# Kernel tuning notes

Hardware: AMD Instinct MI355X
Metric: run time of the kernel (lower is better)

Reference implementation:

```python
import jax, jax.numpy as jnp
import numpy as np

N_NODES = 100000
N_EDGES = 1600000
N_GRAPHS = 64
IN_DIM = 128
HID = 64
N_CLASSES = 10


def setup_inputs() -> dict:
    key = jax.random.key(0)
    ks = jax.random.split(key, 8)
    x = jax.random.normal(ks[0], (N_NODES, IN_DIM), jnp.float32)
    edge_index = jax.random.randint(ks[1], (2, N_EDGES), 0, N_NODES, jnp.int32)
    graph_id = jnp.sort(jax.random.randint(ks[2], (N_NODES,), 0, N_GRAPHS, jnp.int32))
    W1 = jax.random.normal(ks[3], (IN_DIM, HID), jnp.float32) / np.sqrt(IN_DIM)
    b1 = jnp.zeros((HID,), jnp.float32)
    W2 = jax.random.normal(ks[4], (HID, HID), jnp.float32) / np.sqrt(HID)
    b2 = jnp.zeros((HID,), jnp.float32)
    attn_W = jax.random.normal(ks[5], (HID, 1), jnp.float32) / np.sqrt(HID)
    attn_b = jnp.zeros((1,), jnp.float32)
    cls_W = jax.random.normal(ks[6], (HID, N_CLASSES), jnp.float32) / np.sqrt(HID)
    cls_b = jnp.zeros((N_CLASSES,), jnp.float32)
    return {"x": x, "edge_index": edge_index, "graph_id": graph_id,
            "W1": W1, "b1": b1, "W2": W2, "b2": b2,
            "attn_W": attn_W, "attn_b": attn_b, "cls_W": cls_W, "cls_b": cls_b}


def _graph_conv(h, W, b, src, dst, norm_out, norm_in):
    # DGL GraphConv, norm='both': D_in^{-1/2} A D_out^{-1/2} (h W) + b
    h = h @ W                                  # [N, out]
    h = h * norm_out[:, None]                  # scale by src out-degree^{-1/2}
    m = jax.ops.segment_sum(h[src], dst, num_segments=N_NODES)  # SpMM aggregation
    return m * norm_in[:, None] + b


def reference(x, edge_index, graph_id, W1, b1, W2, b2, attn_W, attn_b, cls_W, cls_b):
    src, dst = edge_index[0], edge_index[1]
    ones_e = jnp.ones((src.shape[0],), jnp.float32)
    deg_out = jnp.clip(jax.ops.segment_sum(ones_e, src, num_segments=N_NODES), 1.0)
    deg_in = jnp.clip(jax.ops.segment_sum(ones_e, dst, num_segments=N_NODES), 1.0)
    norm_out = jax.lax.rsqrt(deg_out)
    norm_in = jax.lax.rsqrt(deg_in)

    h = jax.nn.relu(_graph_conv(x, W1, b1, src, dst, norm_out, norm_in))
    h = jax.nn.relu(_graph_conv(h, W2, b2, src, dst, norm_out, norm_in))

    hw = jax.nn.sigmoid(h @ attn_W + attn_b)   # [N, 1] attention gate
    h = h * hw

    # mean_nodes: per-graph mean pooling
    sums = jax.ops.segment_sum(h, graph_id, num_segments=N_GRAPHS)        # [G, HID]
    cnts = jnp.clip(jax.ops.segment_sum(jnp.ones((N_NODES,), jnp.float32), graph_id,
                                        num_segments=N_GRAPHS), 1.0)
    hg = sums / cnts[:, None]
    out = hg @ cls_W + cls_b                   # [G, n_classes]
    return out, hw
```

## Files before the change

kernel.cpp:

```cpp
#include <hip/hip_runtime.h>
#include <stdint.h>


#define N_NODES   100000
#define N_EDGES   1600000
#define N_GRAPHS  64
#define IN_DIM    128
#define HID       64
#define N_CLASSES 10

#define NBUCK     391
#define P1B       196
#define EPB       8192
#define GB_BLOCKS 391
#define MTILES    6250
#define GEMM_BLOCKS 1563
#define SPMM_BLOCKS 3125
#define POOL_SLICES 32
#define WS_NEED   33885952u

typedef __attribute__((ext_vector_type(8))) short short8v;
typedef __attribute__((ext_vector_type(4))) float f32x4;
typedef __bf16 bf16x8 __attribute__((ext_vector_type(8)));

__device__ __forceinline__ f32x4 mfma16(short8v a, short8v b, f32x4 c) {
  return __builtin_amdgcn_mfma_f32_16x16x32_bf16(
      __builtin_bit_cast(bf16x8, a), __builtin_bit_cast(bf16x8, b), c, 0, 0, 0);
}

__device__ __forceinline__ float bf2f(unsigned short u) {
  unsigned int v = ((unsigned int)u) << 16;
  float f;
  __builtin_memcpy(&f, &v, 4);
  return f;
}

__device__ __forceinline__ unsigned short f2bf(float f) {
  unsigned int x;
  __builtin_memcpy(&x, &f, 4);
  unsigned int lsb = (x >> 16) & 1u;
  x += 0x7fffu + lsb;
  return (unsigned short)(x >> 16);
}

__device__ __forceinline__ void unpack_bf2(unsigned int u, float& lo, float& hi) {
  unsigned int a = u << 16;
  unsigned int b = u & 0xffff0000u;
  __builtin_memcpy(&lo, &a, 4);
  __builtin_memcpy(&hi, &b, 4);
}

__device__ __forceinline__ float ldf(const void* p, int i, int mode) {
  return mode ? bf2f(((const unsigned short*)p)[i]) : ((const float*)p)[i];
}

__global__ __launch_bounds__(256) void fallback_kernel(unsigned short* __restrict__ out,
                                                       int n) {
  int i = blockIdx.x * 256 + threadIdx.x;
  if (i < n) out[i] = 0;
}

__global__ __launch_bounds__(256) void wcvt_kernel(
    const unsigned short* __restrict__ xu,
    const void* __restrict__ W1, const void* __restrict__ W2,
    const void* __restrict__ b1, const void* __restrict__ b2,
    const void* __restrict__ attnW, const void* __restrict__ attnb,
    const void* __restrict__ clsW, const void* __restrict__ clsb,
    unsigned short* __restrict__ W1hf, unsigned short* __restrict__ W1lf,
    unsigned short* __restrict__ W2hf, unsigned short* __restrict__ W2lf,
    float* __restrict__ b1f, float* __restrict__ b2f,
    float* __restrict__ attnWf, float* __restrict__ attnbf,
    float* __restrict__ clsWf, float* __restrict__ clsbf,
    int* __restrict__ flag) {
  __shared__ int cnt[4];
  __shared__ int smode;
  int tid = (int)threadIdx.x;
  unsigned u = xu[2 * tid];
  int e = (int)((u >> 7) & 0xFF);
  int ok = (e >= 110 && e <= 132) ? 1 : 0;
  unsigned long long m = __ballot(ok);
  if ((tid & 63) == 0) cnt[tid >> 6] = __popcll(m);
  __syncthreads();
  if (tid == 0) {
    smode = (cnt[0] + cnt[1] + cnt[2] + cnt[3] > 128) ? 1 : 0;
    if (blockIdx.x == 0) {
      flag[0] = smode;
      flag[1] = 1;
    }
  }
  __syncthreads();
  int mode = smode;

  int i = blockIdx.x * 256 + tid;
  if (i < 1024) {
    int tile = i >> 6, lane = i & 63;
    int kt = tile >> 2, ct = tile & 3;
#pragma unroll
    for (int j = 0; j < 8; ++j) {
      int k = kt * 32 + ((lane >> 4) << 3) + j;
      int d = (ct << 4) + (lane & 15);
      float v = ldf(W1, k * HID + d, mode);
      unsigned short h = f2bf(v);
      unsigned short l = f2bf(v - bf2f(h));
      W1hf[i * 8 + j] = h;
      W1lf[i * 8 + j] = l;
    }
  } else if (i < 1536) {
    int ii = i - 1024;
    int tile = ii >> 6, lane = ii & 63;
    int kt = tile >> 2, ct = tile & 3;
#pragma unroll
    for (int j = 0; j < 8; ++j) {
      int k = kt * 32 + ((lane >> 4) << 3) + j;
      int d = (ct << 4) + (lane & 15);
      float v = ldf(W2, k * HID + d, mode);
      unsigned short h = f2bf(v);
      unsigned short l = f2bf(v - bf2f(h));
      W2hf[ii * 8 + j] = h;
      W2lf[ii * 8 + j] = l;
    }
  }
  if (i < HID) {
    b1f[i] = ldf(b1, i, mode);
    b2f[i] = ldf(b2, i, mode);
    attnWf[i] = ldf(attnW, i, mode);
  }
  if (i == 0) attnbf[0] = ldf(attnb, 0, mode);
  if (i < HID * N_CLASSES) clsWf[i] = ldf(clsW, i, mode);
  if (i < N_CLASSES) clsbf[i] = ldf(clsb, i, mode);
}

template <int K, bool SCALE>
__device__ __forceinline__ void gemm_tile(
    const void* __restrict__ A, const unsigned short* __restrict__ Whf,
    const unsigned short* __restrict__ Wlf, const float* __restrict__ norm_out,
    unsigned short* __restrict__ out, int mode, int mtile, int lane) {
  int n0 = mtile << 4;
  int row = lane & 15;
  int kg = lane >> 4;
  f32x4 acc0 = {0.f, 0.f, 0.f, 0.f};
  f32x4 acc1 = {0.f, 0.f, 0.f, 0.f};
  f32x4 acc2 = {0.f, 0.f, 0.f, 0.f};
  f32x4 acc3 = {0.f, 0.f, 0.f, 0.f};
  const short8v* whb0 = (const short8v*)Whf + lane;
  const short8v* wlb0 = (const short8v*)Wlf + lane;
  if (mode) {
    const unsigned short* xr = (const unsigned short*)A + (size_t)(n0 + row) * K + (kg << 3);
#pragma unroll
    for (int kt = 0; kt < K / 32; ++kt) {
      uint4 va = *(const uint4*)(xr + kt * 32);
      short8v xh = __builtin_bit_cast(short8v, va);
      const short8v* wh = whb0 + (size_t)(kt * 4) * 64;
      const short8v* wl = wlb0 + (size_t)(kt * 4) * 64;
      acc0 = mfma16(xh, wh[0], acc0);
      acc1 = mfma16(xh, wh[64], acc1);
      acc2 = mfma16(xh, wh[128], acc2);
      acc3 = mfma16(xh, wh[192], acc3);
      acc0 = mfma16(xh, wl[0], acc0);
      acc1 = mfma16(xh, wl[64], acc1);
      acc2 = mfma16(xh, wl[128], acc2);
      acc3 = mfma16(xh, wl[192], acc3);
    }
  } else {
    const float* xr = (const float*)A + (size_t)(n0 + row) * K + (kg << 3);
#pragma unroll
    for (int kt = 0; kt < K / 32; ++kt) {
      float4 a0 = *(const float4*)(xr + kt * 32);
      float4 a1 = *(const float4*)(xr + kt * 32 + 4);
      float xv[8] = {a0.x, a0.y, a0.z, a0.w, a1.x, a1.y, a1.z, a1.w};
      short8v xh, xl;
#pragma unroll
      for (int j = 0; j < 8; ++j) {
        unsigned short h = f2bf(xv[j]);
        unsigned short l = f2bf(xv[j] - bf2f(h));
        xh[j] = (short)h;
        xl[j] = (short)l;
      }
      const short8v* wh = whb0 + (size_t)(kt * 4) * 64;
      const short8v* wl = wlb0 + (size_t)(kt * 4) * 64;
      acc0 = mfma16(xh, wh[0], acc0);
      acc1 = mfma16(xh, wh[64], acc1);
      acc2 = mfma16(xh, wh[128], acc2);
      acc3 = mfma16(xh, wh[192], acc3);
      acc0 = mfma16(xh, wl[0], acc0);
      acc1 = mfma16(xh, wl[64], acc1);
      acc2 = mfma16(xh, wl[128], acc2);
      acc3 = mfma16(xh, wl[192], acc3);
      acc0 = mfma16(xl, wh[0], acc0);
      acc1 = mfma16(xl, wh[64], acc1);
      acc2 = mfma16(xl, wh[128], acc2);
      acc3 = mfma16(xl, wh[192], acc3);
    }
  }
  int col = lane & 15;
#pragma unroll
  for (int i = 0; i < 4; ++i) {
    int n = n0 + (kg << 2) + i;
    float s = SCALE ? norm_out[n] : 1.f;
    size_t rb = (size_t)n << 6;
    out[rb + col]      = f2bf(acc0[i] * s);
    out[rb + 16 + col] = f2bf(acc1[i] * s);
    out[rb + 32 + col] = f2bf(acc2[i] * s);
    out[rb + 48 + col] = f2bf(acc3[i] * s);
  }
}

__global__ __launch_bounds__(256) void fatA_kernel(
    const int* __restrict__ ei, int* __restrict__ blkhistD,
    int* __restrict__ blkhistS,
    const int* __restrict__ gid, int* __restrict__ gstart,
    const void* __restrict__ x, const unsigned short* __restrict__ W1hf,
    const unsigned short* __restrict__ W1lf, unsigned short* __restrict__ bufA,
    const int* __restrict__ flag) {
  int b = (int)blockIdx.x;
  int t = (int)threadIdx.x;
  if (b < P1B) {
    __shared__ int hD[NBUCK];
    __shared__ int hS[NBUCK];
    for (int i = t; i < NBUCK; i += 256) { hD[i] = 0; hS[i] = 0; }
    __syncthreads();
    int base_e = b * EPB;
    for (int s = 0; s < EPB / 1024; ++s) {
      int e4 = base_e + s * 1024 + t * 4;
      if (e4 < N_EDGES) {
        int4 s4 = *(const int4*)(ei + e4);
        int4 d4 = *(const int4*)(ei + N_EDGES + e4);
        int ss[4] = {s4.x, s4.y, s4.z, s4.w};
        int dd[4] = {d4.x, d4.y, d4.z, d4.w};
#pragma unroll
        for (int j = 0; j < 4; ++j) {
          if ((unsigned)ss[j] < N_NODES) atomicAdd(&hS[ss[j] >> 8], 1);
          if ((unsigned)dd[j] < N_NODES) atomicAdd(&hD[dd[j] >> 8], 1);
        }
      }
    }
    __syncthreads();
    for (int i = t; i < NBUCK; i += 256) {
      blkhistD[i * P1B + b] = hD[i];
      blkhistS[i * P1B + b] = hS[i];
    }
  } else if (b < P1B + GEMM_BLOCKS) {
    int mode = flag[0];
    int mtile = (b - P1B) * 4 + (t >> 6);
    if (mtile < MTILES)
      gemm_tile<IN_DIM, false>(x, W1hf, W1lf, (const float*)0, bufA, mode,
                               mtile, t & 63);
  } else {
    int bb = b - P1B - GEMM_BLOCKS;
    int n = bb * 256 + t;
    if (n >= N_NODES) return;
    int gc = gid[n] & (N_GRAPHS - 1);
    if (n == 0) {
      for (int g = 0; g <= gc; ++g) gstart[g] = 0;
    } else {
      int gp = gid[n - 1] & (N_GRAPHS - 1);
      for (int g = gp + 1; g <= gc; ++g) gstart[g] = n;
    }
    if (n == N_NODES - 1) {
      for (int g = gc + 1; g <= N_GRAPHS; ++g) gstart[g] = N_NODES;
    }
  }
}

__global__ __launch_bounds__(512) void bucket_scan_kernel(
    int* __restrict__ blkhistD, int* __restrict__ blkhistS,
    int* __restrict__ bstart_d, int* __restrict__ bstart_s) {
  int* hist = (blockIdx.x == 0) ? blkhistD : blkhistS;
  int* bst  = (blockIdx.x == 0) ? bstart_d : bstart_s;
  int u = (int)threadIdx.x;
  int tot = 0;
  if (u < NBUCK) {
    const int* row = hist + u * P1B;
    for (int blk = 0; blk < P1B; ++blk) tot += row[blk];
  }
  __shared__ int smA[512];
  __shared__ int smB[512];
  smA[u] = tot;
  __syncthreads();
  int* a = smA;
  int* bq = smB;
  for (int off = 1; off < 512; off <<= 1) {
    int v = a[u];
    if (u >= off) v += a[u - off];
    bq[u] = v;
    __syncthreads();
    int* tmp = a; a = bq; bq = tmp;
  }
  int excl = a[u] - tot;
  if (u <= NBUCK) bst[u] = excl;
  if (u < NBUCK) {
    int off2 = excl;
    int* row = hist + u * P1B;
    for (int blk = 0; blk < P1B; ++blk) {
      int h = row[blk];
      row[blk] = off2;
      off2 += h;
    }
  }
}

__global__ __launch_bounds__(256) void part_scatter_kernel(
    const int* __restrict__ ei, const int* __restrict__ blkbaseD,
    const int* __restrict__ blkbaseS,
    unsigned int* __restrict__ edstP, int* __restrict__ esrc) {
  __shared__ int cD[NBUCK];
  __shared__ int cS[NBUCK];
  int b = (int)blockIdx.x;
  int t = (int)threadIdx.x;
  for (int i = t; i < NBUCK; i += 256) {
    cD[i] = blkbaseD[i * P1B + b];
    cS[i] = blkbaseS[i * P1B + b];
  }
  __syncthreads();
  int base_e = b * EPB;
  for (int s = 0; s < EPB / 1024; ++s) {
    int e4 = base_e + s * 1024 + t * 4;
    if (e4 < N_EDGES) {
      int4 s4 = *(const int4*)(ei + e4);
      int4 d4 = *(const int4*)(ei + N_EDGES + e4);
      int ss[4] = {s4.x, s4.y, s4.z, s4.w};
      int dd[4] = {d4.x, d4.y, d4.z, d4.w};
#pragma unroll
      for (int j = 0; j < 4; ++j) {
        if ((unsigned)ss[j] < N_NODES) {
          int slot = atomicAdd(&cS[ss[j] >> 8], 1);
          esrc[slot] = ss[j];
        }
        if ((unsigned)dd[j] < N_NODES) {
          int slot = atomicAdd(&cD[dd[j] >> 8], 1);
          edstP[slot] = ((unsigned int)ss[j] << 8) | ((unsigned int)dd[j] & 255u);
        }
      }
    }
  }
}

__global__ __launch_bounds__(256) void csr_kernel(
    const unsigned int* __restrict__ edstP, const int* __restrict__ esrc,
    const int* __restrict__ bstart_d, const int* __restrict__ bstart_s,
    int* __restrict__ rowptr, int* __restrict__ colx,
    float* __restrict__ norm_in, float* __restrict__ norm_out) {
  __shared__ int lc[256];
  __shared__ int smA[256];
  __shared__ int smB[256];
  int b = (int)blockIdx.x;
  int t = (int)threadIdx.x;
  if (b < NBUCK) {
    int node0 = b << 8;
    int base = bstart_d[b];
    int end  = bstart_d[b + 1];
    lc[t] = 0;
    __syncthreads();
    for (int i = base + t; i < end; i += 256) {
      unsigned int p = edstP[i];
      atomicAdd(&lc[p & 255u], 1);
    }
    __syncthreads();
    int my = lc[t];
    smA[t] = my;
    __syncthreads();
    int* a = smA;
    int* bq = smB;
    for (int off = 1; off < 256; off <<= 1) {
      int v = a[t];
      if (t >= off) v += a[t - off];
      bq[t] = v;
      __syncthreads();
      int* tmp = a; a = bq; bq = tmp;
    }
    int excl = a[t] - my;
    int n = node0 + t;
    if (n <= N_NODES) rowptr[n] = base + excl;
    if (n < N_NODES) {
      int c = my < 1 ? 1 : my;
      norm_in[n] = rsqrtf((float)c);
    }
    __syncthreads();
    lc[t] = base + excl;
    __syncthreads();
    for (int i = base + t; i < end; i += 256) {
      unsigned int p = edstP[i];
      int slot = atomicAdd(&lc[p & 255u], 1);
      colx[slot] = (int)(p >> 8);
    }
  } else {
    int bb = b - NBUCK;
    int node0 = bb << 8;
    int base = bstart_s[bb];
    int end  = bstart_s[bb + 1];
    lc[t] = 0;
    __syncthreads();
    for (int i = base + t; i < end; i += 256) {
      atomicAdd(&lc[esrc[i] - node0], 1);
    }
    __syncthreads();
    int n = node0 + t;
    if (n < N_NODES) {
      int c = lc[t] < 1 ? 1 : lc[t];
      norm_out[n] = rsqrtf((float)c);
    }
  }
}

template <int K>
__global__ __launch_bounds__(256) void gemm_mfma_kernel(
    const void* __restrict__ A, const unsigned short* __restrict__ Whf,
    const unsigned short* __restrict__ Wlf, const float* __restrict__ norm_out,
    unsigned short* __restrict__ out, const int* __restrict__ flag) {
  int mode = flag[0];
  int mtile = (int)blockIdx.x * 4 + ((int)threadIdx.x >> 6);
  if (mtile >= MTILES) return;
  gemm_tile<K, true>(A, Whf, Wlf, norm_out, out, mode, mtile,
                     (int)threadIdx.x & 63);
}

__device__ __forceinline__ void accum8f(uint4 v, float no, float acc[8]) {
  float lo, hi;
  unpack_bf2(v.x, lo, hi); acc[0] = fmaf(lo, no, acc[0]); acc[1] = fmaf(hi, no, acc[1]);
  unpack_bf2(v.y, lo, hi); acc[2] = fmaf(lo, no, acc[2]); acc[3] = fmaf(hi, no, acc[3]);
  unpack_bf2(v.z, lo, hi); acc[4] = fmaf(lo, no, acc[4]); acc[5] = fmaf(hi, no, acc[5]);
  unpack_bf2(v.w, lo, hi); acc[6] = fmaf(lo, no, acc[6]); acc[7] = fmaf(hi, no, acc[7]);
}

__device__ __forceinline__ void spmm_gather8s(const unsigned short* __restrict__ hs,
                                              const int* __restrict__ col,
                                              const float* __restrict__ no,
                                              int e0, int e1, int dim0,
                                              float acc[8]) {
  int e = e0;
  for (; e + 4 <= e1; e += 4) {
    int c0 = col[e], c1 = col[e + 1], c2 = col[e + 2], c3 = col[e + 3];
    float n0 = no[c0], n1 = no[c1], n2 = no[c2], n3 = no[c3];
    uint4 v0 = *(const uint4*)(hs + ((size_t)c0 << 6) + dim0);
    uint4 v1 = *(const uint4*)(hs + ((size_t)c1 << 6) + dim0);
    uint4 v2 = *(const uint4*)(hs + ((size_t)c2 << 6) + dim0);
    uint4 v3 = *(const uint4*)(hs + ((size_t)c3 << 6) + dim0);
    accum8f(v0, n0, acc);
    accum8f(v1, n1, acc);
    accum8f(v2, n2, acc);
    accum8f(v3, n3, acc);
  }
  for (; e < e1; ++e) {
    int c = col[e];
    uint4 v = *(const uint4*)(hs + ((size_t)c << 6) + dim0);
    accum8f(v, no[c], acc);
  }
}

__device__ __forceinline__ void accum8(uint4 v, float acc[8]) {
  float lo, hi;
  unpack_bf2(v.x, lo, hi); acc[0] += lo; acc[1] += hi;
  unpack_bf2(v.y, lo, hi); acc[2] += lo; acc[3] += hi;
  unpack_bf2(v.z, lo, hi); acc[4] += lo; acc[5] += hi;
  unpack_bf2(v.w, lo, hi); acc[6] += lo; acc[7] += hi;
}

__device__ __forceinline__ void spmm_gather8(const unsigned short* __restrict__ hs,
                                             const int* __restrict__ col,
                                             int e0, int e1, int dim0,
                                             float acc[8]) {
  int e = e0;
  for (; e + 4 <= e1; e += 4) {
    int c0 = col[e], c1 = col[e + 1], c2 = col[e + 2], c3 = col[e + 3];
    uint4 v0 = *(const uint4*)(hs + ((size_t)c0 << 6) + dim0);
    uint4 v1 = *(const uint4*)(hs + ((size_t)c1 << 6) + dim0);
    uint4 v2 = *(const uint4*)(hs + ((size_t)c2 << 6) + dim0);
    uint4 v3 = *(const uint4*)(hs + ((size_t)c3 << 6) + dim0);
    accum8(v0, acc);
    accum8(v1, acc);
    accum8(v2, acc);
    accum8(v3, acc);
  }
  for (; e < e1; ++e) {
    int c = col[e];
    uint4 v = *(const uint4*)(hs + ((size_t)c << 6) + dim0);
    accum8(v, acc);
  }
}

__global__ __launch_bounds__(256) void spmm_kernel(const unsigned short* __restrict__ hs,
                                                   const int* __restrict__ rowptr,
                                                   const int* __restrict__ col,
                                                   const float* __restrict__ norm_out,
                                                   const float* __restrict__ norm_in,
                                                   const float* __restrict__ b1f,
                                                   unsigned short* __restrict__ out) {
  int n = (int)(blockIdx.x * 32 + (threadIdx.x >> 3));
  int dim0 = ((int)threadIdx.x & 7) << 3;
  if (n >= N_NODES) return;
  int e0 = rowptr[n], e1 = rowptr[n + 1];
  if (e0 < 0) e0 = 0;
  if (e1 > N_EDGES) e1 = N_EDGES;
  float acc[8];
#pragma unroll
  for (int i = 0; i < 8; ++i) acc[i] = 0.f;
  spmm_gather8s(hs, col, norm_out, e0, e1, dim0, acc);
  float nin = norm_in[n];
  unsigned int pk[4];
#pragma unroll
  for (int i = 0; i < 4; ++i) {
    float vlo = fmaxf(acc[2 * i] * nin + b1f[dim0 + 2 * i], 0.f);
    float vhi = fmaxf(acc[2 * i + 1] * nin + b1f[dim0 + 2 * i + 1], 0.f);
    pk[i] = (unsigned int)f2bf(vlo) | ((unsigned int)f2bf(vhi) << 16);
  }
  *(uint4*)(out + ((size_t)n << 6) + dim0) = make_uint4(pk[0], pk[1], pk[2], pk[3]);
}

__global__ __launch_bounds__(256) void spmm_attn_kernel(
    const unsigned short* __restrict__ hs,
    const int* __restrict__ rowptr, const int* __restrict__ col,
    const float* __restrict__ norm_in, const float* __restrict__ b2f,
    const float* __restrict__ attnWf, const float* __restrict__ attnbf,
    void* __restrict__ out_base, unsigned short* __restrict__ gated,
    const int* __restrict__ flag) {
  int mode = flag[0];
  int n = (int)(blockIdx.x * 32 + (threadIdx.x >> 3));
  int dim0 = ((int)threadIdx.x & 7) << 3;
  if (n >= N_NODES) return;
  int e0 = rowptr[n], e1 = rowptr[n + 1];
  if (e0 < 0) e0 = 0;
  if (e1 > N_EDGES) e1 = N_EDGES;
  float acc[8];
#pragma unroll
  for (int i = 0; i < 8; ++i) acc[i] = 0.f;
  spmm_gather8(hs, col, e0, e1, dim0, acc);
  float nin = norm_in[n];
  float vv[8];
  float p = 0.f;
#pragma unroll
  for (int i = 0; i < 8; ++i) {
    vv[i] = fmaxf(acc[i] * nin + b2f[dim0 + i], 0.f);
    p += vv[i] * attnWf[dim0 + i];
  }
#pragma unroll
  for (int m = 1; m <= 4; m <<= 1) p += __shfl_xor(p, m, 64);
  float logit = p + attnbf[0];
  float hwv = 1.f / (1.f + __expf(-logit));
  if ((threadIdx.x & 7) == 0) {
    if (mode) ((unsigned short*)out_base)[N_GRAPHS * N_CLASSES + n] = f2bf(hwv);
    else      ((float*)out_base)[N_GRAPHS * N_CLASSES + n] = hwv;
  }
  unsigned int pk[4];
#pragma unroll
  for (int i = 0; i < 4; ++i) {
    pk[i] = (unsigned int)f2bf(vv[2 * i] * hwv) |
            ((unsigned int)f2bf(vv[2 * i + 1] * hwv) << 16);
  }
  *(uint4*)(gated + ((size_t)n << 6) + dim0) = make_uint4(pk[0], pk[1], pk[2], pk[3]);
}

__global__ __launch_bounds__(256) void pool_kernel(const unsigned short* __restrict__ gated,
                                                   const int* __restrict__ gstart,
                                                   float* __restrict__ gpart) {
  int g = (int)blockIdx.x >> 5;
  int s = (int)blockIdx.x & 31;
  int dim = (int)threadIdx.x & 63;
  int rsel = (int)threadIdx.x >> 6;
  int r0 = gstart[g], r1 = gstart[g + 1];
  if (r0 < 0) r0 = 0;
  if (r1 > N_NODES) r1 = N_NODES;
  int len = r1 - r0;
  if (len < 0) len = 0;
  int a = r0 + (int)(((long long)len * s) >> 5);
  int bnd = r0 + (int)(((long long)len * (s + 1)) >> 5);
  float acc = 0.f;
  for (int r = a + rsel; r < bnd; r += 4)
    acc += bf2f(gated[((size_t)r << 6) + dim]);
  __shared__ float sm[256];
  sm[threadIdx.x] = acc;
  __syncthreads();
  if (threadIdx.x < 64)
    gpart[((size_t)blockIdx.x << 6) + dim] =
        sm[dim] + sm[64 + dim] + sm[128 + dim] + sm[192 + dim];
}

__global__ __launch_bounds__(640) void final_kernel(const float* __restrict__ gpart,
                                                    const int* __restrict__ gstart,
                                                    const float* __restrict__ clsWf,
                                                    const float* __restrict__ clsbf,
                                                    void* __restrict__ out_base,
                                                    const int* __restrict__ flag) {
  __shared__ float gs[N_GRAPHS * HID];
  int t = (int)threadIdx.x;
  for (int idx = t; idx < N_GRAPHS * HID; idx += 640) {
    int g = idx >> 6, d = idx & 63;
    float a = 0.f;
#pragma unroll
    for (int s = 0; s < POOL_SLICES; ++s)
      a += gpart[(((size_t)(g << 5) + s) << 6) + d];
    gs[idx] = a;
  }
  __syncthreads();
  int mode = flag[0];
  if (t >= N_GRAPHS * N_CLASSES) return;
  int g = t / N_CLASSES, c = t - g * N_CLASSES;
  int cg = gstart[g + 1] - gstart[g];
  if (cg < 1) cg = 1;
  float inv = 1.f / (float)cg;
  float acc = 0.f;
#pragma unroll
  for (int d = 0; d < HID; ++d) acc += gs[(g << 6) + d] * clsWf[d * N_CLASSES + c];
  float r = acc * inv + clsbf[c];
  if (mode) ((unsigned short*)out_base)[t] = f2bf(r);
  else      ((float*)out_base)[t] = r;
}

extern "C" void kernel_launch(void* const* d_in, const int* in_sizes, int n_in,
                              void* d_out, int out_size, void* d_ws, size_t ws_size,
                              hipStream_t stream) {
  const void* x     = d_in[0];
  const int*  ei    = (const int*)d_in[1];
  const int*  gid   = (const int*)d_in[2];
  const void* W1    = d_in[3];
  const void* b1    = d_in[4];
  const void* W2    = d_in[5];
  const void* b2    = d_in[6];
  const void* attnW = d_in[7];
  const void* attnb = d_in[8];
  const void* clsW  = d_in[9];
  const void* clsb  = d_in[10];

  if (ws_size < (size_t)WS_NEED) {
    fallback_kernel<<<(out_size + 255) / 256, 256, 0, stream>>>(
        (unsigned short*)d_out, out_size);
    return;
  }

  char* w = (char*)d_ws;
  int*   flag     = (int*)(w + 0);
  int*   gstart   = (int*)(w + 64);
  int*   bstart_d = (int*)(w + 16960);
  int*   bstart_s = (int*)(w + 18560);
  int*   blkhD    = (int*)(w + 20160);
  int*   blkhS    = (int*)(w + 326720);
  int*   rowptr   = (int*)(w + 633280);
  float* norm_out = (float*)(w + 1033344);
  float* norm_in  = (float*)(w + 1433344);
  unsigned short* W1hf = (unsigned short*)(w + 1833344);
  unsigned short* W1lf = (unsigned short*)(w + 1849728);
  unsigned short* W2hf = (unsigned short*)(w + 1866112);
  unsigned short* W2lf = (unsigned short*)(w + 1874304);
  float* b1f      = (float*)(w + 1882496);
  float* b2f      = (float*)(w + 1882752);
  float* attnWf   = (float*)(w + 1883008);
  float* attnbf   = (float*)(w + 1883264);
  float* clsWf    = (float*)(w + 1883328);
  float* clsbf    = (float*)(w + 1885888);
  int*   colx     = (int*)(w + 1885952);
  unsigned int* edstP = (unsigned int*)(w + 8285952);
  int*   esrc     = (int*)(w + 14685952);
  unsigned short* bufA = (unsigned short*)(w + 21085952);
  unsigned short* bufB = (unsigned short*)(w + 8285952);
  float* gpart    = (float*)(w + 20160);

  wcvt_kernel<<<32, 256, 0, stream>>>((const unsigned short*)x, W1, W2, b1, b2,
                                      attnW, attnb, clsW, clsb, W1hf, W1lf,
                                      W2hf, W2lf, b1f, b2f, attnWf, attnbf,
                                      clsWf, clsbf, flag);

  fatA_kernel<<<P1B + GEMM_BLOCKS + GB_BLOCKS, 256, 0, stream>>>(
      ei, blkhD, blkhS, gid, gstart, x, W1hf, W1lf, bufA, flag);

  bucket_scan_kernel<<<2, 512, 0, stream>>>(blkhD, blkhS, bstart_d, bstart_s);

  part_scatter_kernel<<<P1B, 256, 0, stream>>>(ei, blkhD, blkhS, edstP, esrc);
  csr_kernel<<<2 * NBUCK, 256, 0, stream>>>(edstP, esrc, bstart_d, bstart_s,
                                            rowptr, colx, norm_in, norm_out);

  spmm_kernel<<<SPMM_BLOCKS, 256, 0, stream>>>(bufA, rowptr, colx, norm_out,
                                               norm_in, b1f, bufB);

  gemm_mfma_kernel<HID><<<GEMM_BLOCKS, 256, 0, stream>>>(
      bufB, W2hf, W2lf, norm_out, bufA, flag + 1);
  spmm_attn_kernel<<<SPMM_BLOCKS, 256, 0, stream>>>(
      bufA, rowptr, colx, norm_in, b2f, attnWf, attnbf, d_out, bufB, flag);

  pool_kernel<<<N_GRAPHS * POOL_SLICES, 256, 0, stream>>>(bufB, gstart, gpart);
  final_kernel<<<1, 640, 0, stream>>>(gpart, gstart, clsWf, clsbf, d_out, flag);
}
```

Before: 283.8 us.

## Fuse layer-1 SpMM with layer-2 GEMM and transpose bucket histogram layout

The first SpMM output tile (32 nodes × 64 dims) now stays in shared memory, and the W2 GEMM runs on it with MFMA in the same block. This removes the intermediate h1 write and reread plus a separate kernel launch. The per-block bucket histograms are also stored block-major, so writes from the histogram kernel and reads in the scatter kernel are coalesced, while the scan kernel reads with stride. The fused GEMM ignores the mode flag (flag+1) the old GEMM kernel used, which may drop a precision path, and it writes bf16 outputs with scattered 2-byte stores.

```diff
diff --git a/kernel.cpp b/kernel.cpp
--- a/kernel.cpp
+++ b/kernel.cpp
@@ -236,8 +236,8 @@
     }
     __syncthreads();
     for (int i = t; i < NBUCK; i += 256) {
-      blkhistD[i * P1B + b] = hD[i];
-      blkhistS[i * P1B + b] = hS[i];
+      blkhistD[b * NBUCK + i] = hD[i];
+      blkhistS[b * NBUCK + i] = hS[i];
     }
   } else if (b < P1B + GEMM_BLOCKS) {
     int mode = flag[0];
@@ -270,8 +270,7 @@
   int u = (int)threadIdx.x;
   int tot = 0;
   if (u < NBUCK) {
-    const int* row = hist + u * P1B;
-    for (int blk = 0; blk < P1B; ++blk) tot += row[blk];
+    for (int blk = 0; blk < P1B; ++blk) tot += hist[blk * NBUCK + u];
   }
   __shared__ int smA[512];
   __shared__ int smB[512];
@@ -290,10 +289,9 @@
   if (u <= NBUCK) bst[u] = excl;
   if (u < NBUCK) {
     int off2 = excl;
-    int* row = hist + u * P1B;
     for (int blk = 0; blk < P1B; ++blk) {
-      int h = row[blk];
-      row[blk] = off2;
+      int h = hist[blk * NBUCK + u];
+      hist[blk * NBUCK + u] = off2;
       off2 += h;
     }
   }
@@ -308,8 +306,8 @@
   int b = (int)blockIdx.x;
   int t = (int)threadIdx.x;
   for (int i = t; i < NBUCK; i += 256) {
-    cD[i] = blkbaseD[i * P1B + b];
-    cS[i] = blkbaseS[i * P1B + b];
+    cD[i] = blkbaseD[b * NBUCK + i];
+    cS[i] = blkbaseS[b * NBUCK + i];
   }
   __syncthreads();
   int base_e = b * EPB;
@@ -400,18 +398,6 @@
       norm_out[n] = rsqrtf((float)c);
     }
   }
-}
-
-template <int K>
-__global__ __launch_bounds__(256) void gemm_mfma_kernel(
-    const void* __restrict__ A, const unsigned short* __restrict__ Whf,
-    const unsigned short* __restrict__ Wlf, const float* __restrict__ norm_out,
-    unsigned short* __restrict__ out, const int* __restrict__ flag) {
-  int mode = flag[0];
-  int mtile = (int)blockIdx.x * 4 + ((int)threadIdx.x >> 6);
-  if (mtile >= MTILES) return;
-  gemm_tile<K, true>(A, Whf, Wlf, norm_out, out, mode, mtile,
-                     (int)threadIdx.x & 63);
 }
 
 __device__ __forceinline__ void accum8f(uint4 v, float no, float acc[8]) {
@@ -478,16 +464,18 @@
   }
 }
 
-__global__ __launch_bounds__(256) void spmm_kernel(const unsigned short* __restrict__ hs,
-                                                   const int* __restrict__ rowptr,
-                                                   const int* __restrict__ col,
-                                                   const float* __restrict__ norm_out,
-                                                   const float* __restrict__ norm_in,
-                                                   const float* __restrict__ b1f,
-                                                   unsigned short* __restrict__ out) {
-  int n = (int)(blockIdx.x * 32 + (threadIdx.x >> 3));
-  int dim0 = ((int)threadIdx.x & 7) << 3;
-  if (n >= N_NODES) return;
+__global__ __launch_bounds__(256) void spmm_gemm_kernel(
+    const unsigned short* __restrict__ hs,
+    const int* __restrict__ rowptr, const int* __restrict__ col,
+    const float* __restrict__ norm_out, const float* __restrict__ norm_in,
+    const float* __restrict__ b1f,
+    const unsigned short* __restrict__ W2hf,
+    const unsigned short* __restrict__ W2lf,
+    unsigned short* __restrict__ hs2) {
+  __shared__ unsigned short h1s[32][72];
+  int t = (int)threadIdx.x;
+  int n = (int)blockIdx.x * 32 + (t >> 3);
+  int dim0 = (t & 7) << 3;
   int e0 = rowptr[n], e1 = rowptr[n + 1];
   if (e0 < 0) e0 = 0;
   if (e1 > N_EDGES) e1 = N_EDGES;
@@ -503,7 +491,34 @@
     float vhi = fmaxf(acc[2 * i + 1] * nin + b1f[dim0 + 2 * i + 1], 0.f);
     pk[i] = (unsigned int)f2bf(vlo) | ((unsigned int)f2bf(vhi) << 16);
   }
-  *(uint4*)(out + ((size_t)n << 6) + dim0) = make_uint4(pk[0], pk[1], pk[2], pk[3]);
+  *(uint4*)&h1s[t >> 3][dim0] = make_uint4(pk[0], pk[1], pk[2], pk[3]);
+  __syncthreads();
+  int wv = t >> 6;
+  int lane = t & 63;
+  int mloc = (wv >> 1) << 4;
+  int ct0 = (wv & 1) << 1;
+  int row = lane & 15, kg = lane >> 4;
+  f32x4 a0 = {0.f, 0.f, 0.f, 0.f};
+  f32x4 a1 = {0.f, 0.f, 0.f, 0.f};
+  const short8v* wh = (const short8v*)W2hf + lane;
+  const short8v* wl = (const short8v*)W2lf + lane;
+#pragma unroll
+  for (int kt = 0; kt < 2; ++kt) {
+    short8v av = *(const short8v*)&h1s[mloc + row][kt * 32 + (kg << 3)];
+    a0 = mfma16(av, wh[(kt * 4 + ct0) * 64], a0);
+    a1 = mfma16(av, wh[(kt * 4 + ct0 + 1) * 64], a1);
+    a0 = mfma16(av, wl[(kt * 4 + ct0) * 64], a0);
+    a1 = mfma16(av, wl[(kt * 4 + ct0 + 1) * 64], a1);
+  }
+  int colc = lane & 15;
+#pragma unroll
+  for (int i = 0; i < 4; ++i) {
+    int ng = (int)blockIdx.x * 32 + mloc + (kg << 2) + i;
+    float s = norm_out[ng];
+    size_t rb = (size_t)ng << 6;
+    hs2[rb + (ct0 << 4) + colc]       = f2bf(a0[i] * s);
+    hs2[rb + ((ct0 + 1) << 4) + colc] = f2bf(a1[i] * s);
+  }
 }
 
 __global__ __launch_bounds__(256) void spmm_attn_kernel(
@@ -662,19 +677,16 @@
       ei, blkhD, blkhS, gid, gstart, x, W1hf, W1lf, bufA, flag);
 
   bucket_scan_kernel<<<2, 512, 0, stream>>>(blkhD, blkhS, bstart_d, bstart_s);
-
   part_scatter_kernel<<<P1B, 256, 0, stream>>>(ei, blkhD, blkhS, edstP, esrc);
   csr_kernel<<<2 * NBUCK, 256, 0, stream>>>(edstP, esrc, bstart_d, bstart_s,
                                             rowptr, colx, norm_in, norm_out);
 
-  spmm_kernel<<<SPMM_BLOCKS, 256, 0, stream>>>(bufA, rowptr, colx, norm_out,
-                                               norm_in, b1f, bufB);
-
-  gemm_mfma_kernel<HID><<<GEMM_BLOCKS, 256, 0, stream>>>(
-      bufB, W2hf, W2lf, norm_out, bufA, flag + 1);
+  spmm_gemm_kernel<<<SPMM_BLOCKS, 256, 0, stream>>>(
+      bufA, rowptr, colx, norm_out, norm_in, b1f, W2hf, W2lf, bufB);
+
   spmm_attn_kernel<<<SPMM_BLOCKS, 256, 0, stream>>>(
-      bufA, rowptr, colx, norm_in, b2f, attnWf, attnbf, d_out, bufB, flag);
-
-  pool_kernel<<<N_GRAPHS * POOL_SLICES, 256, 0, stream>>>(bufB, gstart, gpart);
+      bufB, rowptr, colx, norm_in, b2f, attnWf, attnbf, d_out, bufA, flag);
+
+  pool_kernel<<<N_GRAPHS * POOL_SLICES, 256, 0, stream>>>(bufA, gstart, gpart);
   final_kernel<<<1, 640, 0, stream>>>(gpart, gstart, clsWf, clsbf, d_out, flag);
 }
```

Result: faster. 258.1 us (median of 2 runs) (-9.0%).
